# Performance work log

Measured on AMD Instinct MI355X. Metric: run time of the kernel, lower is better.

The kernel has to match this reference:

```python
import jax, jax.numpy as jnp
import numpy as np

EPS = 1e-8
NHEAD = 4
N_ITER = 3


def _ln(x, g, b):
    mu = jnp.mean(x, axis=-1, keepdims=True)
    var = jnp.var(x, axis=-1, keepdims=True)
    return (x - mu) / jnp.sqrt(var + 1e-5) * g + b


def _forward(inputs, eps, init_mu, init_logvar, Wk, Wv, Wq,
             ln_in_g, ln_in_b, ln_slot_g, ln_slot_b, ln_res_g, ln_res_b,
             gru_Wih, gru_Whh, gru_bih, gru_bhh, mlp_W1, mlp_W2, mlp_b2):
    B, N, _ = inputs.shape
    D = init_mu.shape[-1]
    dh = D // NHEAD
    # reparameterized init of the figure representation  [B, D]
    rep = init_mu + jnp.exp(0.5 * init_logvar) * eps
    x = _ln(inputs, ln_in_g, ln_in_b)
    # [B, H, N, dh]; k is pre-scaled by sqrt(nhead) as in the source
    k = (x @ Wk).reshape(B, N, NHEAD, dh).transpose(0, 2, 1, 3) * (NHEAD ** 0.5)
    v = (x @ Wv).reshape(B, N, NHEAD, dh).transpose(0, 2, 1, 3)

    def step(rep):
        q = (_ln(rep, ln_slot_g, ln_slot_b) @ Wq).reshape(B, NHEAD, dh)
        # sigmoid attention, normalized over the patch dim N
        w = jax.nn.sigmoid(jnp.einsum('bhnd,bhd->bhn', k, q)) + EPS
        w = w / jnp.sum(w, axis=2, keepdims=True)          # [B, H, N]
        att = jnp.einsum('bhn,bhnd->bhd', w, v).reshape(B, D)
        # GRUCell(input=att, hidden=rep)
        gi = att @ gru_Wih.T + gru_bih
        gh = rep @ gru_Whh.T + gru_bhh
        ir, iz, ig = jnp.split(gi, 3, axis=-1)
        hr, hz, hg = jnp.split(gh, 3, axis=-1)
        r = jax.nn.sigmoid(ir + hr)
        z = jax.nn.sigmoid(iz + hz)
        g = jnp.tanh(ig + r * hg)
        new = (1.0 - z) * g + z * rep
        # residual MLP
        new = new + jax.nn.relu(_ln(new, ln_res_g, ln_res_b) @ mlp_W1) @ mlp_W2 + mlp_b2
        return new, w

    for _ in range(N_ITER):
        rep, w = step(rep)
    # approx_implicit_grad: one extra step from a detached latent
    rep, w = step(jax.lax.stop_gradient(rep))
    return rep, jnp.sum(w, axis=1)[..., None]   # ([B, D], [B, N, 1])


def setup_inputs() -> dict:
    key = jax.random.key(0)
    ks = jax.random.split(key, 12)
    B, N, Din, D, H = 128, 4096, 256, 256, 1024
    s = lambda f: 1.0 / np.sqrt(f)
    return {
        'inputs': jax.random.normal(ks[0], (B, N, Din), jnp.float32),
        'eps': jax.random.normal(ks[1], (B, D), jnp.float32),
        'init_mu': jax.random.normal(ks[2], (1, D), jnp.float32) * 0.02,
        'init_logvar': jax.random.normal(ks[3], (1, D), jnp.float32) * 0.02,
        'Wk': jax.random.normal(ks[4], (Din, D), jnp.float32) * s(Din),
        'Wv': jax.random.normal(ks[5], (Din, D), jnp.float32) * s(Din),
        'Wq': jax.random.normal(ks[6], (D, D), jnp.float32) * s(D),
        'ln_in_g': jnp.ones((Din,), jnp.float32),
        'ln_in_b': jnp.zeros((Din,), jnp.float32),
        'ln_slot_g': jnp.ones((D,), jnp.float32),
        'ln_slot_b': jnp.zeros((D,), jnp.float32),
        'ln_res_g': jnp.ones((D,), jnp.float32),
        'ln_res_b': jnp.zeros((D,), jnp.float32),
        'gru_Wih': jax.random.normal(ks[7], (3 * D, D), jnp.float32) * s(D),
        'gru_Whh': jax.random.normal(ks[8], (3 * D, D), jnp.float32) * s(D),
        'gru_bih': jnp.zeros((3 * D,), jnp.float32),
        'gru_bhh': jnp.zeros((3 * D,), jnp.float32),
        'mlp_W1': jax.random.normal(ks[9], (D, H), jnp.float32) * s(D),
        'mlp_W2': jax.random.normal(ks[10], (H, D), jnp.float32) * s(H),
        'mlp_b2': jnp.zeros((D,), jnp.float32),
    }


def reference(inputs, eps, init_mu, init_logvar, Wk, Wv, Wq,
              ln_in_g, ln_in_b, ln_slot_g, ln_slot_b, ln_res_g, ln_res_b,
              gru_Wih, gru_Whh, gru_bih, gru_bhh, mlp_W1, mlp_W2, mlp_b2):
    return _forward(inputs, eps, init_mu, init_logvar, Wk, Wv, Wq,
                    ln_in_g, ln_in_b, ln_slot_g, ln_slot_b, ln_res_g, ln_res_b,
                    gru_Wih, gru_Whh, gru_bih, gru_bhh, mlp_W1, mlp_W2, mlp_b2)
```

## Files before the change

kernel.cpp:

```cpp
#include <hip/hip_runtime.h>
#include <hip/hip_bf16.h>

typedef __attribute__((ext_vector_type(2))) float f32x2;
typedef __attribute__((ext_vector_type(8))) unsigned short ushort8;
typedef __attribute__((ext_vector_type(4))) unsigned short ushort4_t;

#define N_    4096

__device__ inline float bf2f(unsigned short u){
  union{unsigned int i; float f;} c; c.i = ((unsigned int)u)<<16; return c.f;
}
__device__ inline unsigned short f2bf(float f){
  union{float f; unsigned int i;} c; c.f = f;
  unsigned int x = c.i;
  return (unsigned short)((x + 0x7fffu + ((x>>16)&1u)) >> 16);
}
__device__ inline float sigm(float s){ return 1.0f/(1.0f+__expf(-s)); }
__device__ inline f32x2 up2(unsigned int w){
  union{unsigned int i; float f;} lo, hi;
  lo.i = w<<16; hi.i = w & 0xffff0000u;
  f32x2 r; r.x = lo.f; r.y = hi.f; return r;
}

__device__ inline float blkSum(float v, float* s4){
  v += __shfl_xor(v,1);  v += __shfl_xor(v,2);  v += __shfl_xor(v,4);
  v += __shfl_xor(v,8);  v += __shfl_xor(v,16); v += __shfl_xor(v,32);
  int lane = threadIdx.x & 63, w = threadIdx.x >> 6;
  __syncthreads();
  if (lane==0) s4[w] = v;
  __syncthreads();
  return s4[0]+s4[1]+s4[2]+s4[3];
}

__device__ inline float blkSum16(float v, float* s16){
  #pragma unroll
  for(int o=1;o<64;o<<=1) v += __shfl_xor(v,o);
  int lane = threadIdx.x & 63, w = threadIdx.x >> 6;
  __syncthreads();
  if (lane==0) s16[w] = v;
  __syncthreads();
  float r = 0.f;
  #pragma unroll
  for(int i=0;i<16;i++) r += s16[i];
  return r;
}

__global__ __launch_bounds__(256) void k_prep(
    const float* __restrict__ Wv, const float* __restrict__ Wih,
    const float* __restrict__ Whh, const float* __restrict__ W1,
    const float* __restrict__ W2, const float* __restrict__ Wq,
    const float* __restrict__ Wk,
    unsigned short* __restrict__ Wvp, unsigned short* __restrict__ Wip,
    unsigned short* __restrict__ Whp, unsigned short* __restrict__ W1p,
    unsigned short* __restrict__ W2p, unsigned short* __restrict__ Wqp,
    unsigned short* __restrict__ Wkp){
  int e = blockIdx.x*256 + threadIdx.x;
  if (e < 65536){
    int i = e&3, j = (e>>2)&255, pk = e>>10;
    Wvp[e] = f2bf(Wv[(4*pk+i)*256 + j]);
    Wqp[e] = f2bf(Wq[(4*pk+i)*256 + j]);
  }
  if (e < 196608){
    int i = e&3, j2 = e>>2;
    int j = j2 % 768, pk = j2 / 768;
    Wip[e] = f2bf(Wih[j*256 + 4*pk+i]);
    Whp[e] = f2bf(Whh[j*256 + 4*pk+i]);
  }
  {
    int i = e&3, j = (e>>2)&1023, pk = e>>12;
    W1p[e] = f2bf(W1[(4*pk+i)*1024 + j]);
  }
  {
    int i = e&3, j = (e>>2)&255, pk = e>>10;
    W2p[e] = f2bf(W2[(4*pk+i)*256 + j]);
  }
  if (e < 65536){
    int i = e&3, hc = (e>>2)&1023, pd = e>>12;
    int h = hc>>8, c = hc&255;
    Wkp[e] = f2bf(Wk[c*256 + h*64 + 4*pd+i]);
  }
}

__global__ __launch_bounds__(256) void k_init(
    const float* __restrict__ eps, const float* __restrict__ mu0,
    const float* __restrict__ lv0, const float* __restrict__ sg,
    const float* __restrict__ sb, const float* __restrict__ Wq,
    const unsigned short* __restrict__ Wkp,
    float* __restrict__ rep, float* __restrict__ p_out){
  __shared__ float s4[4]; __shared__ float xq[256]; __shared__ float q_s[256];
  int b = blockIdx.x, c = threadIdx.x;
  float r0 = mu0[c] + __expf(0.5f*lv0[c]) * eps[b*256+c];
  rep[b*256+c] = r0;
  float mu = blkSum(r0, s4) * (1.0f/256.0f);
  float df = r0 - mu;
  float var = blkSum(df*df, s4) * (1.0f/256.0f);
  float rs = rsqrtf(var + 1e-5f);
  xq[c] = df*rs*sg[c] + sb[c];
  __syncthreads();
  float a0=0,a1=0,a2=0,a3=0;
  for(int k=0;k<256;k+=4){
    a0 += xq[k  ]*Wq[(k  )*256+c];
    a1 += xq[k+1]*Wq[(k+1)*256+c];
    a2 += xq[k+2]*Wq[(k+2)*256+c];
    a3 += xq[k+3]*Wq[(k+3)*256+c];
  }
  q_s[c] = a0+a1+a2+a3;
  __syncthreads();
  #pragma unroll
  for(int h=0;h<4;h++){
    float acc = 0.f;
    for(int pd=0;pd<16;pd++){
      ushort4_t w4 = *reinterpret_cast<const ushort4_t*>(Wkp + ((size_t)pd*1024 + h*256 + c)*4);
      acc += bf2f(w4.x)*q_s[h*64+4*pd  ] + bf2f(w4.y)*q_s[h*64+4*pd+1]
           + bf2f(w4.z)*q_s[h*64+4*pd+2] + bf2f(w4.w)*q_s[h*64+4*pd+3];
    }
    p_out[b*1024 + h*256 + c] = 2.0f*acc;
  }
}

__global__ __launch_bounds__(1024) void k_lnattn(
    const float* __restrict__ in, const float* __restrict__ g,
    const float* __restrict__ bln, const float* __restrict__ p,
    unsigned short* __restrict__ x,
    float* __restrict__ u_part, float* __restrict__ ws_part){
  __shared__ float u_red[8][1024];
  __shared__ float ws_red[16][4];
  int split = blockIdx.x, b = blockIdx.y;
  int tid = threadIdx.x, wid = tid>>6, lane = tid&63;
  int grp = tid>>5, cl = tid&31;
  const float* pb = p + (size_t)b*1024;
  f32x2 pp2[4][4];
  #pragma unroll
  for(int h=0;h<4;h++){
    float4 pa = *reinterpret_cast<const float4*>(pb + h*256 + cl*8);
    float4 pc = *reinterpret_cast<const float4*>(pb + h*256 + cl*8 + 4);
    pp2[h][0] = f32x2{pa.x,pa.y}; pp2[h][1] = f32x2{pa.z,pa.w};
    pp2[h][2] = f32x2{pc.x,pc.y}; pp2[h][3] = f32x2{pc.z,pc.w};
  }
  float gg[8], bb[8];
  {
    float4 a = *reinterpret_cast<const float4*>(g + cl*8);
    float4 c = *reinterpret_cast<const float4*>(g + cl*8 + 4);
    gg[0]=a.x; gg[1]=a.y; gg[2]=a.z; gg[3]=a.w; gg[4]=c.x; gg[5]=c.y; gg[6]=c.z; gg[7]=c.w;
    a = *reinterpret_cast<const float4*>(bln + cl*8);
    c = *reinterpret_cast<const float4*>(bln + cl*8 + 4);
    bb[0]=a.x; bb[1]=a.y; bb[2]=a.z; bb[3]=a.w; bb[4]=c.x; bb[5]=c.y; bb[6]=c.z; bb[7]=c.w;
  }
  f32x2 u[4][4] = {};
  float wsum[4] = {0,0,0,0};
  const float* inb = in + ((size_t)b*N_ + split*2048)*256;
  unsigned short* xb = x + ((size_t)b*N_ + split*2048)*256;
  for(int it=0; it<32; ++it){
    int r0 = it*64 + grp, r1 = r0 + 32;
    float4 a0 = *reinterpret_cast<const float4*>(inb + (size_t)r0*256 + cl*8);
    float4 c0 = *reinterpret_cast<const float4*>(inb + (size_t)r0*256 + cl*8 + 4);
    float4 a1 = *reinterpret_cast<const float4*>(inb + (size_t)r1*256 + cl*8);
    float4 c1 = *reinterpret_cast<const float4*>(inb + (size_t)r1*256 + cl*8 + 4);
    float sm0 = a0.x+a0.y+a0.z+a0.w + c0.x+c0.y+c0.z+c0.w;
    float sq0 = a0.x*a0.x+a0.y*a0.y+a0.z*a0.z+a0.w*a0.w
              + c0.x*c0.x+c0.y*c0.y+c0.z*c0.z+c0.w*c0.w;
    float sm1 = a1.x+a1.y+a1.z+a1.w + c1.x+c1.y+c1.z+c1.w;
    float sq1 = a1.x*a1.x+a1.y*a1.y+a1.z*a1.z+a1.w*a1.w
              + c1.x*c1.x+c1.y*c1.y+c1.z*c1.z+c1.w*c1.w;
    #pragma unroll
    for(int o=1;o<32;o<<=1){
      sm0 += __shfl_xor(sm0,o); sq0 += __shfl_xor(sq0,o);
      sm1 += __shfl_xor(sm1,o); sq1 += __shfl_xor(sq1,o);
    }
    float mu0 = sm0*(1.0f/256.0f);
    float rs0 = rsqrtf(sq0*(1.0f/256.0f) - mu0*mu0 + 1e-5f);
    float mu1 = sm1*(1.0f/256.0f);
    float rs1 = rsqrtf(sq1*(1.0f/256.0f) - mu1*mu1 + 1e-5f);
    f32x2 px0[4], px1[4];
    px0[0].x=(a0.x-mu0)*rs0*gg[0]+bb[0]; px0[0].y=(a0.y-mu0)*rs0*gg[1]+bb[1];
    px0[1].x=(a0.z-mu0)*rs0*gg[2]+bb[2]; px0[1].y=(a0.w-mu0)*rs0*gg[3]+bb[3];
    px0[2].x=(c0.x-mu0)*rs0*gg[4]+bb[4]; px0[2].y=(c0.y-mu0)*rs0*gg[5]+bb[5];
    px0[3].x=(c0.z-mu0)*rs0*gg[6]+bb[6]; px0[3].y=(c0.w-mu0)*rs0*gg[7]+bb[7];
    px1[0].x=(a1.x-mu1)*rs1*gg[0]+bb[0]; px1[0].y=(a1.y-mu1)*rs1*gg[1]+bb[1];
    px1[1].x=(a1.z-mu1)*rs1*gg[2]+bb[2]; px1[1].y=(a1.w-mu1)*rs1*gg[3]+bb[3];
    px1[2].x=(c1.x-mu1)*rs1*gg[4]+bb[4]; px1[2].y=(c1.y-mu1)*rs1*gg[5]+bb[5];
    px1[3].x=(c1.z-mu1)*rs1*gg[6]+bb[6]; px1[3].y=(c1.w-mu1)*rs1*gg[7]+bb[7];
    ushort8 o8;
    o8[0]=f2bf(px0[0].x); o8[1]=f2bf(px0[0].y); o8[2]=f2bf(px0[1].x); o8[3]=f2bf(px0[1].y);
    o8[4]=f2bf(px0[2].x); o8[5]=f2bf(px0[2].y); o8[6]=f2bf(px0[3].x); o8[7]=f2bf(px0[3].y);
    *reinterpret_cast<ushort8*>(xb + (size_t)r0*256 + cl*8) = o8;
    o8[0]=f2bf(px1[0].x); o8[1]=f2bf(px1[0].y); o8[2]=f2bf(px1[1].x); o8[3]=f2bf(px1[1].y);
    o8[4]=f2bf(px1[2].x); o8[5]=f2bf(px1[2].y); o8[6]=f2bf(px1[3].x); o8[7]=f2bf(px1[3].y);
    *reinterpret_cast<ushort8*>(xb + (size_t)r1*256 + cl*8) = o8;
    float w0[4], w1[4];
    #pragma unroll
    for(int h=0;h<4;h++){
      f32x2 da = px0[0]*pp2[h][0] + px0[2]*pp2[h][2];
      f32x2 db = px0[1]*pp2[h][1] + px0[3]*pp2[h][3];
      da += db;
      float d0 = da.x + da.y;
      f32x2 ea = px1[0]*pp2[h][0] + px1[2]*pp2[h][2];
      f32x2 eb = px1[1]*pp2[h][1] + px1[3]*pp2[h][3];
      ea += eb;
      float d1 = ea.x + ea.y;
      #pragma unroll
      for(int o=1;o<32;o<<=1){ d0 += __shfl_xor(d0,o); d1 += __shfl_xor(d1,o); }
      w0[h] = sigm(d0) + 1e-8f;
      w1[h] = sigm(d1) + 1e-8f;
      wsum[h] += w0[h] + w1[h];
    }
    #pragma unroll
    for(int h=0;h<4;h++){
      f32x2 wa; wa.x = w0[h]; wa.y = w0[h];
      f32x2 wb; wb.x = w1[h]; wb.y = w1[h];
      #pragma unroll
      for(int j=0;j<4;j++){ u[h][j] += wa*px0[j]; u[h][j] += wb*px1[j]; }
    }
  }
  #pragma unroll
  for(int h=0;h<4;h++){
    #pragma unroll
    for(int j=0;j<4;j++){
      u[h][j].x += __shfl_xor(u[h][j].x,32);
      u[h][j].y += __shfl_xor(u[h][j].y,32);
    }
    wsum[h] += __shfl_xor(wsum[h],32);
  }
  if (wid < 8 && lane < 32){
    #pragma unroll
    for(int h=0;h<4;h++){
      float4 a; a.x=u[h][0].x; a.y=u[h][0].y; a.z=u[h][1].x; a.w=u[h][1].y;
      float4 c; c.x=u[h][2].x; c.y=u[h][2].y; c.z=u[h][3].x; c.w=u[h][3].y;
      *reinterpret_cast<float4*>(&u_red[wid][h*256 + cl*8    ]) = a;
      *reinterpret_cast<float4*>(&u_red[wid][h*256 + cl*8 + 4]) = c;
    }
  }
  if (lane==0){
    #pragma unroll
    for(int h=0;h<4;h++) ws_red[wid][h] = wsum[h];
  }
  __syncthreads();
  if (wid >= 8 && lane < 32){
    #pragma unroll
    for(int h=0;h<4;h++){
      float4 a = *reinterpret_cast<const float4*>(&u_red[wid-8][h*256 + cl*8]);
      float4 c = *reinterpret_cast<const float4*>(&u_red[wid-8][h*256 + cl*8 + 4]);
      a.x+=u[h][0].x; a.y+=u[h][0].y; a.z+=u[h][1].x; a.w+=u[h][1].y;
      c.x+=u[h][2].x; c.y+=u[h][2].y; c.z+=u[h][3].x; c.w+=u[h][3].y;
      *reinterpret_cast<float4*>(&u_red[wid-8][h*256 + cl*8    ]) = a;
      *reinterpret_cast<float4*>(&u_red[wid-8][h*256 + cl*8 + 4]) = c;
    }
  }
  __syncthreads();
  {
    float s = 0.f;
    #pragma unroll
    for(int w=0;w<8;w++) s += u_red[w][tid];
    u_part[((size_t)split*128 + b)*1024 + tid] = s;
  }
  if (tid < 4){
    float s = 0.f;
    #pragma unroll
    for(int w=0;w<16;w++) s += ws_red[w][tid];
    ws_part[((size_t)split*128 + b)*4 + tid] = s;
  }
}

__global__ __launch_bounds__(1024) void k_attnstep(
    const unsigned short* __restrict__ x,
    const float* __restrict__ u_in, const float* __restrict__ ws_in,
    const float* __restrict__ rep_in, float* __restrict__ rep_out,
    const unsigned short* __restrict__ Wvp, const unsigned short* __restrict__ Wip,
    const unsigned short* __restrict__ Whp, const float* __restrict__ bih,
    const float* __restrict__ bhh, const float* __restrict__ ln_rg,
    const float* __restrict__ ln_rb, const unsigned short* __restrict__ W1p,
    const unsigned short* __restrict__ W2p, const float* __restrict__ b2,
    const float* __restrict__ ln_sg, const float* __restrict__ ln_sb,
    const unsigned short* __restrict__ Wqp, const unsigned short* __restrict__ Wkp,
    float* __restrict__ u_out, float* __restrict__ ws_out,
    float* __restrict__ w_buf, int write_w){
  __shared__ float u_s[1024];
  __shared__ float att_s[256], rep_s[256], ln_s[256], nw_s[256], q_s[256];
  __shared__ float gi_s[768], gh_s[768];
  __shared__ float h1_s[1024], p_s[1024], red_a[1024];
  __shared__ float ws_s[4]; __shared__ float s16[16];
  __shared__ float u_red[8][1024];
  __shared__ float ws_red[16][4];
  int split = blockIdx.x, b = blockIdx.y;
  int tid = threadIdx.x;
  int c = tid & 255, s = tid >> 8;
  {
    u_s[tid] = u_in[(size_t)b*1024 + tid] + u_in[((size_t)128 + b)*1024 + tid];
    if (tid < 4) ws_s[tid] = ws_in[b*4 + tid] + ws_in[(128 + b)*4 + tid];
    if (tid < 256) rep_s[tid] = rep_in[b*256 + tid];
  }
  __syncthreads();
  {
    const float* uh = u_s + (c>>6)*256;
    float a0 = 0.f, a1 = 0.f;
    for(int pk=s*16; pk<s*16+16; pk+=2){
      ushort4_t wa = *reinterpret_cast<const ushort4_t*>(Wvp + ((size_t)pk*256 + c)*4);
      ushort4_t wb = *reinterpret_cast<const ushort4_t*>(Wvp + ((size_t)(pk+1)*256 + c)*4);
      a0 += bf2f(wa.x)*uh[4*pk] + bf2f(wa.y)*uh[4*pk+1]
          + bf2f(wa.z)*uh[4*pk+2] + bf2f(wa.w)*uh[4*pk+3];
      a1 += bf2f(wb.x)*uh[4*pk+4] + bf2f(wb.y)*uh[4*pk+5]
          + bf2f(wb.z)*uh[4*pk+6] + bf2f(wb.w)*uh[4*pk+7];
    }
    red_a[tid] = a0+a1;
  }
  __syncthreads();
  if (tid < 256) att_s[tid] = (red_a[tid]+red_a[256+tid]+red_a[512+tid]+red_a[768+tid]) / ws_s[tid>>6];
  __syncthreads();
  if (tid < 768){
    float gi0=0.f, gi1=0.f, gh0=0.f, gh1=0.f;
    for(int pk=0;pk<64;pk+=2){
      ushort4_t wi0 = *reinterpret_cast<const ushort4_t*>(Wip + ((size_t)pk*768 + tid)*4);
      ushort4_t wh0 = *reinterpret_cast<const ushort4_t*>(Whp + ((size_t)pk*768 + tid)*4);
      ushort4_t wi1 = *reinterpret_cast<const ushort4_t*>(Wip + ((size_t)(pk+1)*768 + tid)*4);
      ushort4_t wh1 = *reinterpret_cast<const ushort4_t*>(Whp + ((size_t)(pk+1)*768 + tid)*4);
      gi0 += bf2f(wi0.x)*att_s[4*pk] + bf2f(wi0.y)*att_s[4*pk+1]
           + bf2f(wi0.z)*att_s[4*pk+2] + bf2f(wi0.w)*att_s[4*pk+3];
      gh0 += bf2f(wh0.x)*rep_s[4*pk] + bf2f(wh0.y)*rep_s[4*pk+1]
           + bf2f(wh0.z)*rep_s[4*pk+2] + bf2f(wh0.w)*rep_s[4*pk+3];
      gi1 += bf2f(wi1.x)*att_s[4*pk+4] + bf2f(wi1.y)*att_s[4*pk+5]
           + bf2f(wi1.z)*att_s[4*pk+6] + bf2f(wi1.w)*att_s[4*pk+7];
      gh1 += bf2f(wh1.x)*rep_s[4*pk+4] + bf2f(wh1.y)*rep_s[4*pk+5]
           + bf2f(wh1.z)*rep_s[4*pk+6] + bf2f(wh1.w)*rep_s[4*pk+7];
    }
    gi_s[tid] = gi0+gi1 + bih[tid];
    gh_s[tid] = gh0+gh1 + bhh[tid];
  }
  __syncthreads();
  if (tid < 256){
    float rr = sigm(gi_s[tid]     + gh_s[tid]);
    float zz = sigm(gi_s[256+tid] + gh_s[256+tid]);
    float t3 = tanhf(gi_s[512+tid] + rr*gh_s[512+tid]);
    nw_s[tid] = (1.f-zz)*t3 + zz*rep_s[tid];
  }
  __syncthreads();
  {
    float v = nw_s[c];
    float mu = blkSum16(v, s16)*(1.0f/1024.0f);
    float df = v - mu;
    float var = blkSum16(df*df, s16)*(1.0f/1024.0f);
    float rs = rsqrtf(var+1e-5f);
    if (s==0) ln_s[c] = df*rs*ln_rg[c]+ln_rb[c];
  }
  __syncthreads();
  {
    float a0 = 0.f, a1 = 0.f;
    for(int pk=0;pk<64;pk+=2){
      ushort4_t wa = *reinterpret_cast<const ushort4_t*>(W1p + ((size_t)pk*1024 + tid)*4);
      ushort4_t wb = *reinterpret_cast<const ushort4_t*>(W1p + ((size_t)(pk+1)*1024 + tid)*4);
      a0 += bf2f(wa.x)*ln_s[4*pk] + bf2f(wa.y)*ln_s[4*pk+1]
          + bf2f(wa.z)*ln_s[4*pk+2] + bf2f(wa.w)*ln_s[4*pk+3];
      a1 += bf2f(wb.x)*ln_s[4*pk+4] + bf2f(wb.y)*ln_s[4*pk+5]
          + bf2f(wb.z)*ln_s[4*pk+6] + bf2f(wb.w)*ln_s[4*pk+7];
    }
    h1_s[tid] = fmaxf(a0+a1, 0.f);
  }
  __syncthreads();
  {
    float a0 = 0.f, a1 = 0.f;
    for(int pk=s*64; pk<s*64+64; pk+=2){
      ushort4_t wa = *reinterpret_cast<const ushort4_t*>(W2p + ((size_t)pk*256 + c)*4);
      ushort4_t wb = *reinterpret_cast<const ushort4_t*>(W2p + ((size_t)(pk+1)*256 + c)*4);
      a0 += bf2f(wa.x)*h1_s[4*pk] + bf2f(wa.y)*h1_s[4*pk+1]
          + bf2f(wa.z)*h1_s[4*pk+2] + bf2f(wa.w)*h1_s[4*pk+3];
      a1 += bf2f(wb.x)*h1_s[4*pk+4] + bf2f(wb.y)*h1_s[4*pk+5]
          + bf2f(wb.z)*h1_s[4*pk+6] + bf2f(wb.w)*h1_s[4*pk+7];
    }
    red_a[tid] = a0+a1;
  }
  __syncthreads();
  if (tid < 256){
    float rn = nw_s[tid] + (red_a[tid]+red_a[256+tid]+red_a[512+tid]+red_a[768+tid]) + b2[tid];
    nw_s[tid] = rn;
    if (split==0) rep_out[b*256+tid] = rn;
  }
  __syncthreads();
  {
    float v = nw_s[c];
    float mu = blkSum16(v, s16)*(1.0f/1024.0f);
    float df = v - mu;
    float var = blkSum16(df*df, s16)*(1.0f/1024.0f);
    float rs = rsqrtf(var+1e-5f);
    if (s==0) ln_s[c] = df*rs*ln_sg[c]+ln_sb[c];
  }
  __syncthreads();
  {
    float a0 = 0.f, a1 = 0.f;
    for(int pk=s*16; pk<s*16+16; pk+=2){
      ushort4_t wa = *reinterpret_cast<const ushort4_t*>(Wqp + ((size_t)pk*256 + c)*4);
      ushort4_t wb = *reinterpret_cast<const ushort4_t*>(Wqp + ((size_t)(pk+1)*256 + c)*4);
      a0 += bf2f(wa.x)*ln_s[4*pk] + bf2f(wa.y)*ln_s[4*pk+1]
          + bf2f(wa.z)*ln_s[4*pk+2] + bf2f(wa.w)*ln_s[4*pk+3];
      a1 += bf2f(wb.x)*ln_s[4*pk+4] + bf2f(wb.y)*ln_s[4*pk+5]
          + bf2f(wb.z)*ln_s[4*pk+6] + bf2f(wb.w)*ln_s[4*pk+7];
    }
    red_a[tid] = a0+a1;
  }
  __syncthreads();
  if (tid < 256) q_s[tid] = red_a[tid]+red_a[256+tid]+red_a[512+tid]+red_a[768+tid];
  __syncthreads();
  {
    int h = tid>>8;
    float a0 = 0.f, a1 = 0.f;
    for(int pd=0;pd<16;pd+=2){
      ushort4_t wa = *reinterpret_cast<const ushort4_t*>(Wkp + ((size_t)pd*1024 + tid)*4);
      ushort4_t wb = *reinterpret_cast<const ushort4_t*>(Wkp + ((size_t)(pd+1)*1024 + tid)*4);
      a0 += bf2f(wa.x)*q_s[h*64+4*pd] + bf2f(wa.y)*q_s[h*64+4*pd+1]
          + bf2f(wa.z)*q_s[h*64+4*pd+2] + bf2f(wa.w)*q_s[h*64+4*pd+3];
      a1 += bf2f(wb.x)*q_s[h*64+4*pd+4] + bf2f(wb.y)*q_s[h*64+4*pd+5]
          + bf2f(wb.z)*q_s[h*64+4*pd+6] + bf2f(wb.w)*q_s[h*64+4*pd+7];
    }
    p_s[tid] = 2.0f*(a0+a1);
  }
  __syncthreads();
  int wid = tid>>6, lane = tid&63;
  int grp = tid>>5, cl = tid&31;
  f32x2 pp2[4][4];
  #pragma unroll
  for(int h=0;h<4;h++)
    #pragma unroll
    for(int j2=0;j2<4;j2++){
      pp2[h][j2].x = p_s[h*256 + cl*8 + j2*2];
      pp2[h][j2].y = p_s[h*256 + cl*8 + j2*2 + 1];
    }
  f32x2 u2[4][4] = {};
  float wsum[4] = {0,0,0,0};
  const unsigned short* xb = x + ((size_t)b*N_ + split*2048)*256;
  for(int it=0; it<32; ++it){
    int r0 = it*64 + grp, r1 = r0 + 32;
    uint4 xa = *reinterpret_cast<const uint4*>(xb + (size_t)r0*256 + cl*8);
    uint4 xc = *reinterpret_cast<const uint4*>(xb + (size_t)r1*256 + cl*8);
    f32x2 x0[4], x1[4];
    x0[0]=up2(xa.x); x0[1]=up2(xa.y); x0[2]=up2(xa.z); x0[3]=up2(xa.w);
    x1[0]=up2(xc.x); x1[1]=up2(xc.y); x1[2]=up2(xc.z); x1[3]=up2(xc.w);
    float w0[4], w1[4];
    #pragma unroll
    for(int h=0;h<4;h++){
      f32x2 da = x0[0]*pp2[h][0] + x0[2]*pp2[h][2];
      f32x2 db = x0[1]*pp2[h][1] + x0[3]*pp2[h][3];
      da += db;
      float d0 = da.x + da.y;
      f32x2 ea = x1[0]*pp2[h][0] + x1[2]*pp2[h][2];
      f32x2 eb = x1[1]*pp2[h][1] + x1[3]*pp2[h][3];
      ea += eb;
      float d1 = ea.x + ea.y;
      #pragma unroll
      for(int o=1;o<32;o<<=1){ d0 += __shfl_xor(d0,o); d1 += __shfl_xor(d1,o); }
      w0[h] = sigm(d0) + 1e-8f;
      w1[h] = sigm(d1) + 1e-8f;
      wsum[h] += w0[h] + w1[h];
    }
    #pragma unroll
    for(int h=0;h<4;h++){
      f32x2 wa; wa.x = w0[h]; wa.y = w0[h];
      f32x2 wb; wb.x = w1[h]; wb.y = w1[h];
      #pragma unroll
      for(int j2=0;j2<4;j2++){ u2[h][j2] += wa*x0[j2]; u2[h][j2] += wb*x1[j2]; }
    }
    if (write_w && cl==0){
      float4 wv; wv.x=w0[0]; wv.y=w0[1]; wv.z=w0[2]; wv.w=w0[3];
      *reinterpret_cast<float4*>(w_buf + ((size_t)b*N_ + split*2048 + r0)*4) = wv;
      float4 wz; wz.x=w1[0]; wz.y=w1[1]; wz.z=w1[2]; wz.w=w1[3];
      *reinterpret_cast<float4*>(w_buf + ((size_t)b*N_ + split*2048 + r1)*4) = wz;
    }
  }
  #pragma unroll
  for(int h=0;h<4;h++){
    #pragma unroll
    for(int j2=0;j2<4;j2++){
      u2[h][j2].x += __shfl_xor(u2[h][j2].x,32);
      u2[h][j2].y += __shfl_xor(u2[h][j2].y,32);
    }
    wsum[h] += __shfl_xor(wsum[h],32);
  }
  __syncthreads();
  if (wid < 8 && lane < 32){
    #pragma unroll
    for(int h=0;h<4;h++){
      float4 a; a.x=u2[h][0].x; a.y=u2[h][0].y; a.z=u2[h][1].x; a.w=u2[h][1].y;
      float4 cc; cc.x=u2[h][2].x; cc.y=u2[h][2].y; cc.z=u2[h][3].x; cc.w=u2[h][3].y;
      *reinterpret_cast<float4*>(&u_red[wid][h*256 + cl*8    ]) = a;
      *reinterpret_cast<float4*>(&u_red[wid][h*256 + cl*8 + 4]) = cc;
    }
  }
  if (lane==0){
    #pragma unroll
    for(int h=0;h<4;h++) ws_red[wid][h] = wsum[h];
  }
  __syncthreads();
  if (wid >= 8 && lane < 32){
    #pragma unroll
    for(int h=0;h<4;h++){
      float4 a = *reinterpret_cast<const float4*>(&u_red[wid-8][h*256 + cl*8]);
      float4 cc = *reinterpret_cast<const float4*>(&u_red[wid-8][h*256 + cl*8 + 4]);
      a.x+=u2[h][0].x; a.y+=u2[h][0].y; a.z+=u2[h][1].x; a.w+=u2[h][1].y;
      cc.x+=u2[h][2].x; cc.y+=u2[h][2].y; cc.z+=u2[h][3].x; cc.w+=u2[h][3].y;
      *reinterpret_cast<float4*>(&u_red[wid-8][h*256 + cl*8    ]) = a;
      *reinterpret_cast<float4*>(&u_red[wid-8][h*256 + cl*8 + 4]) = cc;
    }
  }
  __syncthreads();
  {
    float sm = 0.f;
    #pragma unroll
    for(int w=0;w<8;w++) sm += u_red[w][tid];
    u_out[((size_t)split*128 + b)*1024 + tid] = sm;
  }
  if (tid < 4){
    float sm = 0.f;
    #pragma unroll
    for(int w=0;w<16;w++) sm += ws_red[w][tid];
    ws_out[((size_t)split*128 + b)*4 + tid] = sm;
  }
}

__global__ __launch_bounds__(1024) void k_finstep(
    const float* __restrict__ u_in, const float* __restrict__ ws_in,
    const float* __restrict__ rep_in,
    const unsigned short* __restrict__ Wvp, const unsigned short* __restrict__ Wip,
    const unsigned short* __restrict__ Whp, const float* __restrict__ bih,
    const float* __restrict__ bhh, const float* __restrict__ ln_rg,
    const float* __restrict__ ln_rb, const unsigned short* __restrict__ W1p,
    const unsigned short* __restrict__ W2p, const float* __restrict__ b2,
    float* __restrict__ out_rep, float* __restrict__ wsum_tot){
  __shared__ float u_s[1024];
  __shared__ float att_s[256], rep_s[256], ln_s[256], nw_s[256];
  __shared__ float gi_s[768], gh_s[768];
  __shared__ float h1_s[1024], red_a[1024];
  __shared__ float ws_s[4]; __shared__ float s16[16];
  int b = blockIdx.x;
  int tid = threadIdx.x;
  int c = tid & 255, s = tid >> 8;
  {
    u_s[tid] = u_in[(size_t)b*1024 + tid] + u_in[((size_t)128 + b)*1024 + tid];
    if (tid < 4){
      float w = ws_in[b*4 + tid] + ws_in[(128 + b)*4 + tid];
      ws_s[tid] = w; wsum_tot[b*4 + tid] = w;
    }
    if (tid < 256) rep_s[tid] = rep_in[b*256 + tid];
  }
  __syncthreads();
  {
    const float* uh = u_s + (c>>6)*256;
    float a0 = 0.f, a1 = 0.f;
    for(int pk=s*16; pk<s*16+16; pk+=2){
      ushort4_t wa = *reinterpret_cast<const ushort4_t*>(Wvp + ((size_t)pk*256 + c)*4);
      ushort4_t wb = *reinterpret_cast<const ushort4_t*>(Wvp + ((size_t)(pk+1)*256 + c)*4);
      a0 += bf2f(wa.x)*uh[4*pk] + bf2f(wa.y)*uh[4*pk+1]
          + bf2f(wa.z)*uh[4*pk+2] + bf2f(wa.w)*uh[4*pk+3];
      a1 += bf2f(wb.x)*uh[4*pk+4] + bf2f(wb.y)*uh[4*pk+5]
          + bf2f(wb.z)*uh[4*pk+6] + bf2f(wb.w)*uh[4*pk+7];
    }
    red_a[tid] = a0+a1;
  }
  __syncthreads();
  if (tid < 256) att_s[tid] = (red_a[tid]+red_a[256+tid]+red_a[512+tid]+red_a[768+tid]) / ws_s[tid>>6];
  __syncthreads();
  if (tid < 768){
    float gi0=0.f, gi1=0.f, gh0=0.f, gh1=0.f;
    for(int pk=0;pk<64;pk+=2){
      ushort4_t wi0 = *reinterpret_cast<const ushort4_t*>(Wip + ((size_t)pk*768 + tid)*4);
      ushort4_t wh0 = *reinterpret_cast<const ushort4_t*>(Whp + ((size_t)pk*768 + tid)*4);
      ushort4_t wi1 = *reinterpret_cast<const ushort4_t*>(Wip + ((size_t)(pk+1)*768 + tid)*4);
      ushort4_t wh1 = *reinterpret_cast<const ushort4_t*>(Whp + ((size_t)(pk+1)*768 + tid)*4);
      gi0 += bf2f(wi0.x)*att_s[4*pk] + bf2f(wi0.y)*att_s[4*pk+1]
           + bf2f(wi0.z)*att_s[4*pk+2] + bf2f(wi0.w)*att_s[4*pk+3];
      gh0 += bf2f(wh0.x)*rep_s[4*pk] + bf2f(wh0.y)*rep_s[4*pk+1]
           + bf2f(wh0.z)*rep_s[4*pk+2] + bf2f(wh0.w)*rep_s[4*pk+3];
      gi1 += bf2f(wi1.x)*att_s[4*pk+4] + bf2f(wi1.y)*att_s[4*pk+5]
           + bf2f(wi1.z)*att_s[4*pk+6] + bf2f(wi1.w)*att_s[4*pk+7];
      gh1 += bf2f(wh1.x)*rep_s[4*pk+4] + bf2f(wh1.y)*rep_s[4*pk+5]
           + bf2f(wh1.z)*rep_s[4*pk+6] + bf2f(wh1.w)*rep_s[4*pk+7];
    }
    gi_s[tid] = gi0+gi1 + bih[tid];
    gh_s[tid] = gh0+gh1 + bhh[tid];
  }
  __syncthreads();
  if (tid < 256){
    float rr = sigm(gi_s[tid]     + gh_s[tid]);
    float zz = sigm(gi_s[256+tid] + gh_s[256+tid]);
    float t3 = tanhf(gi_s[512+tid] + rr*gh_s[512+tid]);
    nw_s[tid] = (1.f-zz)*t3 + zz*rep_s[tid];
  }
  __syncthreads();
  {
    float v = nw_s[c];
    float mu = blkSum16(v, s16)*(1.0f/1024.0f);
    float df = v - mu;
    float var = blkSum16(df*df, s16)*(1.0f/1024.0f);
    float rs = rsqrtf(var+1e-5f);
    if (s==0) ln_s[c] = df*rs*ln_rg[c]+ln_rb[c];
  }
  __syncthreads();
  {
    float a0 = 0.f, a1 = 0.f;
    for(int pk=0;pk<64;pk+=2){
      ushort4_t wa = *reinterpret_cast<const ushort4_t*>(W1p + ((size_t)pk*1024 + tid)*4);
      ushort4_t wb = *reinterpret_cast<const ushort4_t*>(W1p + ((size_t)(pk+1)*1024 + tid)*4);
      a0 += bf2f(wa.x)*ln_s[4*pk] + bf2f(wa.y)*ln_s[4*pk+1]
          + bf2f(wa.z)*ln_s[4*pk+2] + bf2f(wa.w)*ln_s[4*pk+3];
      a1 += bf2f(wb.x)*ln_s[4*pk+4] + bf2f(wb.y)*ln_s[4*pk+5]
          + bf2f(wb.z)*ln_s[4*pk+6] + bf2f(wb.w)*ln_s[4*pk+7];
    }
    h1_s[tid] = fmaxf(a0+a1, 0.f);
  }
  __syncthreads();
  {
    float a0 = 0.f, a1 = 0.f;
    for(int pk=s*64; pk<s*64+64; pk+=2){
      ushort4_t wa = *reinterpret_cast<const ushort4_t*>(W2p + ((size_t)pk*256 + c)*4);
      ushort4_t wb = *reinterpret_cast<const ushort4_t*>(W2p + ((size_t)(pk+1)*256 + c)*4);
      a0 += bf2f(wa.x)*h1_s[4*pk] + bf2f(wa.y)*h1_s[4*pk+1]
          + bf2f(wa.z)*h1_s[4*pk+2] + bf2f(wa.w)*h1_s[4*pk+3];
      a1 += bf2f(wb.x)*h1_s[4*pk+4] + bf2f(wb.y)*h1_s[4*pk+5]
          + bf2f(wb.z)*h1_s[4*pk+6] + bf2f(wb.w)*h1_s[4*pk+7];
    }
    red_a[tid] = a0+a1;
  }
  __syncthreads();
  if (tid < 256){
    float rn = nw_s[tid] + (red_a[tid]+red_a[256+tid]+red_a[512+tid]+red_a[768+tid]) + b2[tid];
    out_rep[b*256+tid] = rn;
  }
}

__global__ __launch_bounds__(256) void k_wout(
    const float* __restrict__ w_buf, const float* __restrict__ wsum_tot,
    float* __restrict__ out){
  int idx = blockIdx.x*256 + threadIdx.x;
  int b = idx>>12;
  float4 w4 = *reinterpret_cast<const float4*>(w_buf + (size_t)idx*4);
  out[idx] = w4.x/wsum_tot[b*4+0] + w4.y/wsum_tot[b*4+1]
           + w4.z/wsum_tot[b*4+2] + w4.w/wsum_tot[b*4+3];
}

extern "C" void kernel_launch(void* const* d_in, const int* in_sizes, int n_in,
                              void* d_out, int out_size, void* d_ws, size_t ws_size,
                              hipStream_t stream){
  const float* inputs  = (const float*)d_in[0];
  const float* eps     = (const float*)d_in[1];
  const float* init_mu = (const float*)d_in[2];
  const float* init_lv = (const float*)d_in[3];
  const float* Wk      = (const float*)d_in[4];
  const float* Wv      = (const float*)d_in[5];
  const float* Wq      = (const float*)d_in[6];
  const float* ln_in_g = (const float*)d_in[7];
  const float* ln_in_b = (const float*)d_in[8];
  const float* ln_sg   = (const float*)d_in[9];
  const float* ln_sb   = (const float*)d_in[10];
  const float* ln_rg   = (const float*)d_in[11];
  const float* ln_rb   = (const float*)d_in[12];
  const float* Wih     = (const float*)d_in[13];
  const float* Whh     = (const float*)d_in[14];
  const float* bih     = (const float*)d_in[15];
  const float* bhh     = (const float*)d_in[16];
  const float* W1      = (const float*)d_in[17];
  const float* W2      = (const float*)d_in[18];
  const float* b2      = (const float*)d_in[19];

  char* ws = (char*)d_ws;
  size_t off = 0;
  auto alloc = [&](size_t bytes)->void*{
    void* p = ws + off; off += (bytes + 255) & ~(size_t)255; return p;
  };
  unsigned short* x   = (unsigned short*)alloc((size_t)128*N_*256*2);
  unsigned short* Wvp = (unsigned short*)alloc(65536*2);
  unsigned short* Wip = (unsigned short*)alloc(196608*2);
  unsigned short* Whp = (unsigned short*)alloc(196608*2);
  unsigned short* W1p = (unsigned short*)alloc(262144*2);
  unsigned short* W2p = (unsigned short*)alloc(262144*2);
  unsigned short* Wqp = (unsigned short*)alloc(65536*2);
  unsigned short* Wkp = (unsigned short*)alloc(65536*2);
  float* p0    = (float*)alloc((size_t)128*1024*4);
  float* uA    = (float*)alloc((size_t)2*128*1024*4);
  float* uB    = (float*)alloc((size_t)2*128*1024*4);
  float* wsA   = (float*)alloc(2*128*4*4);
  float* wsB   = (float*)alloc(2*128*4*4);
  float* repA  = (float*)alloc(128*256*4);
  float* repB  = (float*)alloc(128*256*4);
  float* wsum_tot = (float*)alloc(512*4);
  float* w_buf = (float*)alloc((size_t)128*N_*4*4);

  float* out_rep = (float*)d_out;
  float* out_w   = out_rep + 128*256;

  k_prep<<<1024,256,0,stream>>>(Wv,Wih,Whh,W1,W2,Wq,Wk, Wvp,Wip,Whp,W1p,W2p,Wqp,Wkp);
  k_init<<<128,256,0,stream>>>(eps, init_mu, init_lv, ln_sg, ln_sb, Wq, Wkp, repA, p0);
  k_lnattn<<<dim3(2,128),1024,0,stream>>>(inputs, ln_in_g, ln_in_b, p0, x, uA, wsA);
  k_attnstep<<<dim3(2,128),1024,0,stream>>>(x, uA, wsA, repA, repB,
      Wvp,Wip,Whp,bih,bhh,ln_rg,ln_rb,W1p,W2p,b2,ln_sg,ln_sb,Wqp,Wkp,
      uB, wsB, w_buf, 0);
  k_attnstep<<<dim3(2,128),1024,0,stream>>>(x, uB, wsB, repB, repA,
      Wvp,Wip,Whp,bih,bhh,ln_rg,ln_rb,W1p,W2p,b2,ln_sg,ln_sb,Wqp,Wkp,
      uA, wsA, w_buf, 0);
  k_attnstep<<<dim3(2,128),1024,0,stream>>>(x, uA, wsA, repA, repB,
      Wvp,Wip,Whp,bih,bhh,ln_rg,ln_rb,W1p,W2p,b2,ln_sg,ln_sb,Wqp,Wkp,
      uB, wsB, w_buf, 1);
  k_finstep<<<128,1024,0,stream>>>(uB, wsB, repB,
      Wvp,Wip,Whp,bih,bhh,ln_rg,ln_rb,W1p,W2p,b2, out_rep, wsum_tot);
  k_wout<<<2048,256,0,stream>>>(w_buf, wsum_tot, out_w);
}
```

Baseline: 616.3 us.

## Use MFMA bf16 for attention logits and split input LayerNorm into own kernel

```diff
diff --git a/kernel.cpp b/kernel.cpp
--- a/kernel.cpp
+++ b/kernel.cpp
@@ -2,6 +2,8 @@
 #include <hip/hip_bf16.h>
 
 typedef __attribute__((ext_vector_type(2))) float f32x2;
+typedef __attribute__((ext_vector_type(4))) float f32x4;
+typedef __attribute__((ext_vector_type(8))) short short8;
 typedef __attribute__((ext_vector_type(8))) unsigned short ushort8;
 typedef __attribute__((ext_vector_type(4))) unsigned short ushort4_t;
 
@@ -118,151 +120,35 @@
   }
 }
 
-__global__ __launch_bounds__(1024) void k_lnattn(
+__global__ __launch_bounds__(256) void k_ln(
     const float* __restrict__ in, const float* __restrict__ g,
-    const float* __restrict__ bln, const float* __restrict__ p,
-    unsigned short* __restrict__ x,
-    float* __restrict__ u_part, float* __restrict__ ws_part){
-  __shared__ float u_red[8][1024];
-  __shared__ float ws_red[16][4];
-  int split = blockIdx.x, b = blockIdx.y;
-  int tid = threadIdx.x, wid = tid>>6, lane = tid&63;
-  int grp = tid>>5, cl = tid&31;
-  const float* pb = p + (size_t)b*1024;
-  f32x2 pp2[4][4];
-  #pragma unroll
-  for(int h=0;h<4;h++){
-    float4 pa = *reinterpret_cast<const float4*>(pb + h*256 + cl*8);
-    float4 pc = *reinterpret_cast<const float4*>(pb + h*256 + cl*8 + 4);
-    pp2[h][0] = f32x2{pa.x,pa.y}; pp2[h][1] = f32x2{pa.z,pa.w};
-    pp2[h][2] = f32x2{pc.x,pc.y}; pp2[h][3] = f32x2{pc.z,pc.w};
-  }
-  float gg[8], bb[8];
-  {
-    float4 a = *reinterpret_cast<const float4*>(g + cl*8);
-    float4 c = *reinterpret_cast<const float4*>(g + cl*8 + 4);
-    gg[0]=a.x; gg[1]=a.y; gg[2]=a.z; gg[3]=a.w; gg[4]=c.x; gg[5]=c.y; gg[6]=c.z; gg[7]=c.w;
-    a = *reinterpret_cast<const float4*>(bln + cl*8);
-    c = *reinterpret_cast<const float4*>(bln + cl*8 + 4);
-    bb[0]=a.x; bb[1]=a.y; bb[2]=a.z; bb[3]=a.w; bb[4]=c.x; bb[5]=c.y; bb[6]=c.z; bb[7]=c.w;
-  }
-  f32x2 u[4][4] = {};
-  float wsum[4] = {0,0,0,0};
-  const float* inb = in + ((size_t)b*N_ + split*2048)*256;
-  unsigned short* xb = x + ((size_t)b*N_ + split*2048)*256;
-  for(int it=0; it<32; ++it){
-    int r0 = it*64 + grp, r1 = r0 + 32;
-    float4 a0 = *reinterpret_cast<const float4*>(inb + (size_t)r0*256 + cl*8);
-    float4 c0 = *reinterpret_cast<const float4*>(inb + (size_t)r0*256 + cl*8 + 4);
-    float4 a1 = *reinterpret_cast<const float4*>(inb + (size_t)r1*256 + cl*8);
-    float4 c1 = *reinterpret_cast<const float4*>(inb + (size_t)r1*256 + cl*8 + 4);
-    float sm0 = a0.x+a0.y+a0.z+a0.w + c0.x+c0.y+c0.z+c0.w;
-    float sq0 = a0.x*a0.x+a0.y*a0.y+a0.z*a0.z+a0.w*a0.w
-              + c0.x*c0.x+c0.y*c0.y+c0.z*c0.z+c0.w*c0.w;
-    float sm1 = a1.x+a1.y+a1.z+a1.w + c1.x+c1.y+c1.z+c1.w;
-    float sq1 = a1.x*a1.x+a1.y*a1.y+a1.z*a1.z+a1.w*a1.w
-              + c1.x*c1.x+c1.y*c1.y+c1.z*c1.z+c1.w*c1.w;
+    const float* __restrict__ bln, unsigned short* __restrict__ x){
+  int wgid = blockIdx.x*4 + (threadIdx.x>>6);
+  int lane = threadIdx.x & 63;
+  float4 gg = reinterpret_cast<const float4*>(g)[lane];
+  float4 bb = reinterpret_cast<const float4*>(bln)[lane];
+  size_t row0 = (size_t)wgid*64;
+  for(int rr=0; rr<64; ++rr){
+    size_t row = row0 + rr;
+    float4 v = reinterpret_cast<const float4*>(in + row*256)[lane];
+    float sm = v.x+v.y+v.z+v.w;
+    float sq = v.x*v.x+v.y*v.y+v.z*v.z+v.w*v.w;
     #pragma unroll
-    for(int o=1;o<32;o<<=1){
-      sm0 += __shfl_xor(sm0,o); sq0 += __shfl_xor(sq0,o);
-      sm1 += __shfl_xor(sm1,o); sq1 += __shfl_xor(sq1,o);
-    }
-    float mu0 = sm0*(1.0f/256.0f);
-    float rs0 = rsqrtf(sq0*(1.0f/256.0f) - mu0*mu0 + 1e-5f);
-    float mu1 = sm1*(1.0f/256.0f);
-    float rs1 = rsqrtf(sq1*(1.0f/256.0f) - mu1*mu1 + 1e-5f);
-    f32x2 px0[4], px1[4];
-    px0[0].x=(a0.x-mu0)*rs0*gg[0]+bb[0]; px0[0].y=(a0.y-mu0)*rs0*gg[1]+bb[1];
-    px0[1].x=(a0.z-mu0)*rs0*gg[2]+bb[2]; px0[1].y=(a0.w-mu0)*rs0*gg[3]+bb[3];
-    px0[2].x=(c0.x-mu0)*rs0*gg[4]+bb[4]; px0[2].y=(c0.y-mu0)*rs0*gg[5]+bb[5];
-    px0[3].x=(c0.z-mu0)*rs0*gg[6]+bb[6]; px0[3].y=(c0.w-mu0)*rs0*gg[7]+bb[7];
-    px1[0].x=(a1.x-mu1)*rs1*gg[0]+bb[0]; px1[0].y=(a1.y-mu1)*rs1*gg[1]+bb[1];
-    px1[1].x=(a1.z-mu1)*rs1*gg[2]+bb[2]; px1[1].y=(a1.w-mu1)*rs1*gg[3]+bb[3];
-    px1[2].x=(c1.x-mu1)*rs1*gg[4]+bb[4]; px1[2].y=(c1.y-mu1)*rs1*gg[5]+bb[5];
-    px1[3].x=(c1.z-mu1)*rs1*gg[6]+bb[6]; px1[3].y=(c1.w-mu1)*rs1*gg[7]+bb[7];
-    ushort8 o8;
-    o8[0]=f2bf(px0[0].x); o8[1]=f2bf(px0[0].y); o8[2]=f2bf(px0[1].x); o8[3]=f2bf(px0[1].y);
-    o8[4]=f2bf(px0[2].x); o8[5]=f2bf(px0[2].y); o8[6]=f2bf(px0[3].x); o8[7]=f2bf(px0[3].y);
-    *reinterpret_cast<ushort8*>(xb + (size_t)r0*256 + cl*8) = o8;
-    o8[0]=f2bf(px1[0].x); o8[1]=f2bf(px1[0].y); o8[2]=f2bf(px1[1].x); o8[3]=f2bf(px1[1].y);
-    o8[4]=f2bf(px1[2].x); o8[5]=f2bf(px1[2].y); o8[6]=f2bf(px1[3].x); o8[7]=f2bf(px1[3].y);
-    *reinterpret_cast<ushort8*>(xb + (size_t)r1*256 + cl*8) = o8;
-    float w0[4], w1[4];
-    #pragma unroll
-    for(int h=0;h<4;h++){
-      f32x2 da = px0[0]*pp2[h][0] + px0[2]*pp2[h][2];
-      f32x2 db = px0[1]*pp2[h][1] + px0[3]*pp2[h][3];
-      da += db;
-      float d0 = da.x + da.y;
-      f32x2 ea = px1[0]*pp2[h][0] + px1[2]*pp2[h][2];
-      f32x2 eb = px1[1]*pp2[h][1] + px1[3]*pp2[h][3];
-      ea += eb;
-      float d1 = ea.x + ea.y;
-      #pragma unroll
-      for(int o=1;o<32;o<<=1){ d0 += __shfl_xor(d0,o); d1 += __shfl_xor(d1,o); }
-      w0[h] = sigm(d0) + 1e-8f;
-      w1[h] = sigm(d1) + 1e-8f;
-      wsum[h] += w0[h] + w1[h];
-    }
-    #pragma unroll
-    for(int h=0;h<4;h++){
-      f32x2 wa; wa.x = w0[h]; wa.y = w0[h];
-      f32x2 wb; wb.x = w1[h]; wb.y = w1[h];
-      #pragma unroll
-      for(int j=0;j<4;j++){ u[h][j] += wa*px0[j]; u[h][j] += wb*px1[j]; }
-    }
-  }
-  #pragma unroll
-  for(int h=0;h<4;h++){
-    #pragma unroll
-    for(int j=0;j<4;j++){
-      u[h][j].x += __shfl_xor(u[h][j].x,32);
-      u[h][j].y += __shfl_xor(u[h][j].y,32);
-    }
-    wsum[h] += __shfl_xor(wsum[h],32);
-  }
-  if (wid < 8 && lane < 32){
-    #pragma unroll
-    for(int h=0;h<4;h++){
-      float4 a; a.x=u[h][0].x; a.y=u[h][0].y; a.z=u[h][1].x; a.w=u[h][1].y;
-      float4 c; c.x=u[h][2].x; c.y=u[h][2].y; c.z=u[h][3].x; c.w=u[h][3].y;
-      *reinterpret_cast<float4*>(&u_red[wid][h*256 + cl*8    ]) = a;
-      *reinterpret_cast<float4*>(&u_red[wid][h*256 + cl*8 + 4]) = c;
-    }
-  }
-  if (lane==0){
-    #pragma unroll
-    for(int h=0;h<4;h++) ws_red[wid][h] = wsum[h];
-  }
-  __syncthreads();
-  if (wid >= 8 && lane < 32){
-    #pragma unroll
-    for(int h=0;h<4;h++){
-      float4 a = *reinterpret_cast<const float4*>(&u_red[wid-8][h*256 + cl*8]);
-      float4 c = *reinterpret_cast<const float4*>(&u_red[wid-8][h*256 + cl*8 + 4]);
-      a.x+=u[h][0].x; a.y+=u[h][0].y; a.z+=u[h][1].x; a.w+=u[h][1].y;
-      c.x+=u[h][2].x; c.y+=u[h][2].y; c.z+=u[h][3].x; c.w+=u[h][3].y;
-      *reinterpret_cast<float4*>(&u_red[wid-8][h*256 + cl*8    ]) = a;
-      *reinterpret_cast<float4*>(&u_red[wid-8][h*256 + cl*8 + 4]) = c;
-    }
-  }
-  __syncthreads();
-  {
-    float s = 0.f;
-    #pragma unroll
-    for(int w=0;w<8;w++) s += u_red[w][tid];
-    u_part[((size_t)split*128 + b)*1024 + tid] = s;
-  }
-  if (tid < 4){
-    float s = 0.f;
-    #pragma unroll
-    for(int w=0;w<16;w++) s += ws_red[w][tid];
-    ws_part[((size_t)split*128 + b)*4 + tid] = s;
+    for(int o=1;o<64;o<<=1){ sm += __shfl_xor(sm,o); sq += __shfl_xor(sq,o); }
+    float mu = sm*(1.0f/256.0f);
+    float var = sq*(1.0f/256.0f) - mu*mu;
+    float rs = rsqrtf(var + 1e-5f);
+    ushort4_t o4;
+    o4.x = f2bf((v.x-mu)*rs*gg.x + bb.x);
+    o4.y = f2bf((v.y-mu)*rs*gg.y + bb.y);
+    o4.z = f2bf((v.z-mu)*rs*gg.z + bb.z);
+    o4.w = f2bf((v.w-mu)*rs*gg.w + bb.w);
+    reinterpret_cast<ushort4_t*>(x + row*256)[lane] = o4;
   }
 }
 
 __global__ __launch_bounds__(1024) void k_attnstep(
-    const unsigned short* __restrict__ x,
+    const unsigned short* __restrict__ x, const float* __restrict__ p_buf,
     const float* __restrict__ u_in, const float* __restrict__ ws_in,
     const float* __restrict__ rep_in, float* __restrict__ rep_out,
     const unsigned short* __restrict__ Wvp, const unsigned short* __restrict__ Wip,
@@ -273,238 +159,252 @@
     const float* __restrict__ ln_sg, const float* __restrict__ ln_sb,
     const unsigned short* __restrict__ Wqp, const unsigned short* __restrict__ Wkp,
     float* __restrict__ u_out, float* __restrict__ ws_out,
-    float* __restrict__ w_buf, int write_w){
+    float* __restrict__ w_buf, int write_w, int first){
   __shared__ float u_s[1024];
-  __shared__ float att_s[256], rep_s[256], ln_s[256], nw_s[256], q_s[256];
+  __shared__ float att_s[256], rep_s[256], ln_s[256], nw_s[256];
   __shared__ float gi_s[768], gh_s[768];
   __shared__ float h1_s[1024], p_s[1024], red_a[1024];
   __shared__ float ws_s[4]; __shared__ float s16[16];
-  __shared__ float u_red[8][1024];
+  __shared__ unsigned short pT[16*264];
+  __shared__ float w_lds[16][32][4];
+  __shared__ float u_red[4][1024];
   __shared__ float ws_red[16][4];
   int split = blockIdx.x, b = blockIdx.y;
   int tid = threadIdx.x;
   int c = tid & 255, s = tid >> 8;
-  {
+  if (!first){
     u_s[tid] = u_in[(size_t)b*1024 + tid] + u_in[((size_t)128 + b)*1024 + tid];
     if (tid < 4) ws_s[tid] = ws_in[b*4 + tid] + ws_in[(128 + b)*4 + tid];
     if (tid < 256) rep_s[tid] = rep_in[b*256 + tid];
-  }
-  __syncthreads();
-  {
-    const float* uh = u_s + (c>>6)*256;
-    float a0 = 0.f, a1 = 0.f;
-    for(int pk=s*16; pk<s*16+16; pk+=2){
-      ushort4_t wa = *reinterpret_cast<const ushort4_t*>(Wvp + ((size_t)pk*256 + c)*4);
-      ushort4_t wb = *reinterpret_cast<const ushort4_t*>(Wvp + ((size_t)(pk+1)*256 + c)*4);
-      a0 += bf2f(wa.x)*uh[4*pk] + bf2f(wa.y)*uh[4*pk+1]
-          + bf2f(wa.z)*uh[4*pk+2] + bf2f(wa.w)*uh[4*pk+3];
-      a1 += bf2f(wb.x)*uh[4*pk+4] + bf2f(wb.y)*uh[4*pk+5]
-          + bf2f(wb.z)*uh[4*pk+6] + bf2f(wb.w)*uh[4*pk+7];
-    }
-    red_a[tid] = a0+a1;
-  }
-  __syncthreads();
-  if (tid < 256) att_s[tid] = (red_a[tid]+red_a[256+tid]+red_a[512+tid]+red_a[768+tid]) / ws_s[tid>>6];
-  __syncthreads();
-  if (tid < 768){
-    float gi0=0.f, gi1=0.f, gh0=0.f, gh1=0.f;
-    for(int pk=0;pk<64;pk+=2){
-      ushort4_t wi0 = *reinterpret_cast<const ushort4_t*>(Wip + ((size_t)pk*768 + tid)*4);
-      ushort4_t wh0 = *reinterpret_cast<const ushort4_t*>(Whp + ((size_t)pk*768 + tid)*4);
-      ushort4_t wi1 = *reinterpret_cast<const ushort4_t*>(Wip + ((size_t)(pk+1)*768 + tid)*4);
-      ushort4_t wh1 = *reinterpret_cast<const ushort4_t*>(Whp + ((size_t)(pk+1)*768 + tid)*4);
-      gi0 += bf2f(wi0.x)*att_s[4*pk] + bf2f(wi0.y)*att_s[4*pk+1]
-           + bf2f(wi0.z)*att_s[4*pk+2] + bf2f(wi0.w)*att_s[4*pk+3];
-      gh0 += bf2f(wh0.x)*rep_s[4*pk] + bf2f(wh0.y)*rep_s[4*pk+1]
-           + bf2f(wh0.z)*rep_s[4*pk+2] + bf2f(wh0.w)*rep_s[4*pk+3];
-      gi1 += bf2f(wi1.x)*att_s[4*pk+4] + bf2f(wi1.y)*att_s[4*pk+5]
-           + bf2f(wi1.z)*att_s[4*pk+6] + bf2f(wi1.w)*att_s[4*pk+7];
-      gh1 += bf2f(wh1.x)*rep_s[4*pk+4] + bf2f(wh1.y)*rep_s[4*pk+5]
-           + bf2f(wh1.z)*rep_s[4*pk+6] + bf2f(wh1.w)*rep_s[4*pk+7];
-    }
-    gi_s[tid] = gi0+gi1 + bih[tid];
-    gh_s[tid] = gh0+gh1 + bhh[tid];
-  }
-  __syncthreads();
-  if (tid < 256){
-    float rr = sigm(gi_s[tid]     + gh_s[tid]);
-    float zz = sigm(gi_s[256+tid] + gh_s[256+tid]);
-    float t3 = tanhf(gi_s[512+tid] + rr*gh_s[512+tid]);
-    nw_s[tid] = (1.f-zz)*t3 + zz*rep_s[tid];
-  }
-  __syncthreads();
-  {
-    float v = nw_s[c];
-    float mu = blkSum16(v, s16)*(1.0f/1024.0f);
-    float df = v - mu;
-    float var = blkSum16(df*df, s16)*(1.0f/1024.0f);
-    float rs = rsqrtf(var+1e-5f);
-    if (s==0) ln_s[c] = df*rs*ln_rg[c]+ln_rb[c];
-  }
-  __syncthreads();
-  {
-    float a0 = 0.f, a1 = 0.f;
-    for(int pk=0;pk<64;pk+=2){
-      ushort4_t wa = *reinterpret_cast<const ushort4_t*>(W1p + ((size_t)pk*1024 + tid)*4);
-      ushort4_t wb = *reinterpret_cast<const ushort4_t*>(W1p + ((size_t)(pk+1)*1024 + tid)*4);
-      a0 += bf2f(wa.x)*ln_s[4*pk] + bf2f(wa.y)*ln_s[4*pk+1]
-          + bf2f(wa.z)*ln_s[4*pk+2] + bf2f(wa.w)*ln_s[4*pk+3];
-      a1 += bf2f(wb.x)*ln_s[4*pk+4] + bf2f(wb.y)*ln_s[4*pk+5]
-          + bf2f(wb.z)*ln_s[4*pk+6] + bf2f(wb.w)*ln_s[4*pk+7];
-    }
-    h1_s[tid] = fmaxf(a0+a1, 0.f);
-  }
-  __syncthreads();
-  {
-    float a0 = 0.f, a1 = 0.f;
-    for(int pk=s*64; pk<s*64+64; pk+=2){
-      ushort4_t wa = *reinterpret_cast<const ushort4_t*>(W2p + ((size_t)pk*256 + c)*4);
-      ushort4_t wb = *reinterpret_cast<const ushort4_t*>(W2p + ((size_t)(pk+1)*256 + c)*4);
-      a0 += bf2f(wa.x)*h1_s[4*pk] + bf2f(wa.y)*h1_s[4*pk+1]
-          + bf2f(wa.z)*h1_s[4*pk+2] + bf2f(wa.w)*h1_s[4*pk+3];
-      a1 += bf2f(wb.x)*h1_s[4*pk+4] + bf2f(wb.y)*h1_s[4*pk+5]
-          + bf2f(wb.z)*h1_s[4*pk+6] + bf2f(wb.w)*h1_s[4*pk+7];
-    }
-    red_a[tid] = a0+a1;
-  }
-  __syncthreads();
-  if (tid < 256){
-    float rn = nw_s[tid] + (red_a[tid]+red_a[256+tid]+red_a[512+tid]+red_a[768+tid]) + b2[tid];
-    nw_s[tid] = rn;
-    if (split==0) rep_out[b*256+tid] = rn;
-  }
-  __syncthreads();
-  {
-    float v = nw_s[c];
-    float mu = blkSum16(v, s16)*(1.0f/1024.0f);
-    float df = v - mu;
-    float var = blkSum16(df*df, s16)*(1.0f/1024.0f);
-    float rs = rsqrtf(var+1e-5f);
-    if (s==0) ln_s[c] = df*rs*ln_sg[c]+ln_sb[c];
-  }
-  __syncthreads();
-  {
-    float a0 = 0.f, a1 = 0.f;
-    for(int pk=s*16; pk<s*16+16; pk+=2){
-      ushort4_t wa = *reinterpret_cast<const ushort4_t*>(Wqp + ((size_t)pk*256 + c)*4);
-      ushort4_t wb = *reinterpret_cast<const ushort4_t*>(Wqp + ((size_t)(pk+1)*256 + c)*4);
-      a0 += bf2f(wa.x)*ln_s[4*pk] + bf2f(wa.y)*ln_s[4*pk+1]
-          + bf2f(wa.z)*ln_s[4*pk+2] + bf2f(wa.w)*ln_s[4*pk+3];
-      a1 += bf2f(wb.x)*ln_s[4*pk+4] + bf2f(wb.y)*ln_s[4*pk+5]
-          + bf2f(wb.z)*ln_s[4*pk+6] + bf2f(wb.w)*ln_s[4*pk+7];
-    }
-    red_a[tid] = a0+a1;
-  }
-  __syncthreads();
-  if (tid < 256) q_s[tid] = red_a[tid]+red_a[256+tid]+red_a[512+tid]+red_a[768+tid];
-  __syncthreads();
-  {
-    int h = tid>>8;
-    float a0 = 0.f, a1 = 0.f;
-    for(int pd=0;pd<16;pd+=2){
-      ushort4_t wa = *reinterpret_cast<const ushort4_t*>(Wkp + ((size_t)pd*1024 + tid)*4);
-      ushort4_t wb = *reinterpret_cast<const ushort4_t*>(Wkp + ((size_t)(pd+1)*1024 + tid)*4);
-      a0 += bf2f(wa.x)*q_s[h*64+4*pd] + bf2f(wa.y)*q_s[h*64+4*pd+1]
-          + bf2f(wa.z)*q_s[h*64+4*pd+2] + bf2f(wa.w)*q_s[h*64+4*pd+3];
-      a1 += bf2f(wb.x)*q_s[h*64+4*pd+4] + bf2f(wb.y)*q_s[h*64+4*pd+5]
-          + bf2f(wb.z)*q_s[h*64+4*pd+6] + bf2f(wb.w)*q_s[h*64+4*pd+7];
-    }
-    p_s[tid] = 2.0f*(a0+a1);
-  }
-  __syncthreads();
-  int wid = tid>>6, lane = tid&63;
-  int grp = tid>>5, cl = tid&31;
-  f32x2 pp2[4][4];
+    __syncthreads();
+    {
+      const float* uh = u_s + (c>>6)*256;
+      float a0 = 0.f, a1 = 0.f;
+      for(int pk=s*16; pk<s*16+16; pk+=2){
+        ushort4_t wa = *reinterpret_cast<const ushort4_t*>(Wvp + ((size_t)pk*256 + c)*4);
+        ushort4_t wb = *reinterpret_cast<const ushort4_t*>(Wvp + ((size_t)(pk+1)*256 + c)*4);
+        a0 += bf2f(wa.x)*uh[4*pk] + bf2f(wa.y)*uh[4*pk+1]
+            + bf2f(wa.z)*uh[4*pk+2] + bf2f(wa.w)*uh[4*pk+3];
+        a1 += bf2f(wb.x)*uh[4*pk+4] + bf2f(wb.y)*uh[4*pk+5]
+            + bf2f(wb.z)*uh[4*pk+6] + bf2f(wb.w)*uh[4*pk+7];
+      }
+      red_a[tid] = a0+a1;
+    }
+    __syncthreads();
+    if (tid < 256) att_s[tid] = (red_a[tid]+red_a[256+tid]+red_a[512+tid]+red_a[768+tid]) / ws_s[tid>>6];
+    __syncthreads();
+    if (tid < 768){
+      float gi0=0.f, gi1=0.f, gh0=0.f, gh1=0.f;
+      for(int pk=0;pk<64;pk+=2){
+        ushort4_t wi0 = *reinterpret_cast<const ushort4_t*>(Wip + ((size_t)pk*768 + tid)*4);
+        ushort4_t wh0 = *reinterpret_cast<const ushort4_t*>(Whp + ((size_t)pk*768 + tid)*4);
+        ushort4_t wi1 = *reinterpret_cast<const ushort4_t*>(Wip + ((size_t)(pk+1)*768 + tid)*4);
+        ushort4_t wh1 = *reinterpret_cast<const ushort4_t*>(Whp + ((size_t)(pk+1)*768 + tid)*4);
+        gi0 += bf2f(wi0.x)*att_s[4*pk] + bf2f(wi0.y)*att_s[4*pk+1]
+             + bf2f(wi0.z)*att_s[4*pk+2] + bf2f(wi0.w)*att_s[4*pk+3];
+        gh0 += bf2f(wh0.x)*rep_s[4*pk] + bf2f(wh0.y)*rep_s[4*pk+1]
+             + bf2f(wh0.z)*rep_s[4*pk+2] + bf2f(wh0.w)*rep_s[4*pk+3];
+        gi1 += bf2f(wi1.x)*att_s[4*pk+4] + bf2f(wi1.y)*att_s[4*pk+5]
+             + bf2f(wi1.z)*att_s[4*pk+6] + bf2f(wi1.w)*att_s[4*pk+7];
+        gh1 += bf2f(wh1.x)*rep_s[4*pk+4] + bf2f(wh1.y)*rep_s[4*pk+5]
+             + bf2f(wh1.z)*rep_s[4*pk+6] + bf2f(wh1.w)*rep_s[4*pk+7];
+      }
+      gi_s[tid] = gi0+gi1 + bih[tid];
+      gh_s[tid] = gh0+gh1 + bhh[tid];
+    }
+    __syncthreads();
+    if (tid < 256){
+      float rr = sigm(gi_s[tid]     + gh_s[tid]);
+      float zz = sigm(gi_s[256+tid] + gh_s[256+tid]);
+      float t3 = tanhf(gi_s[512+tid] + rr*gh_s[512+tid]);
+      nw_s[tid] = (1.f-zz)*t3 + zz*rep_s[tid];
+    }
+    __syncthreads();
+    {
+      float v = nw_s[c];
+      float mu = blkSum16(v, s16)*(1.0f/1024.0f);
+      float df = v - mu;
+      float var = blkSum16(df*df, s16)*(1.0f/1024.0f);
+      float rs = rsqrtf(var+1e-5f);
+      if (s==0) ln_s[c] = df*rs*ln_rg[c]+ln_rb[c];
+    }
+    __syncthreads();
+    {
+      float a0 = 0.f, a1 = 0.f;
+      for(int pk=0;pk<64;pk+=2){
+        ushort4_t wa = *reinterpret_cast<const ushort4_t*>(W1p + ((size_t)pk*1024 + tid)*4);
+        ushort4_t wb = *reinterpret_cast<const ushort4_t*>(W1p + ((size_t)(pk+1)*1024 + tid)*4);
+        a0 += bf2f(wa.x)*ln_s[4*pk] + bf2f(wa.y)*ln_s[4*pk+1]
+            + bf2f(wa.z)*ln_s[4*pk+2] + bf2f(wa.w)*ln_s[4*pk+3];
+        a1 += bf2f(wb.x)*ln_s[4*pk+4] + bf2f(wb.y)*ln_s[4*pk+5]
+            + bf2f(wb.z)*ln_s[4*pk+6] + bf2f(wb.w)*ln_s[4*pk+7];
+      }
+      h1_s[tid] = fmaxf(a0+a1, 0.f);
+    }
+    __syncthreads();
+    {
+      float a0 = 0.f, a1 = 0.f;
+      for(int pk=s*64; pk<s*64+64; pk+=2){
+        ushort4_t wa = *reinterpret_cast<const ushort4_t*>(W2p + ((size_t)pk*256 + c)*4);
+        ushort4_t wb = *reinterpret_cast<const ushort4_t*>(W2p + ((size_t)(pk+1)*256 + c)*4);
+        a0 += bf2f(wa.x)*h1_s[4*pk] + bf2f(wa.y)*h1_s[4*pk+1]
+            + bf2f(wa.z)*h1_s[4*pk+2] + bf2f(wa.w)*h1_s[4*pk+3];
+        a1 += bf2f(wb.x)*h1_s[4*pk+4] + bf2f(wb.y)*h1_s[4*pk+5]
+            + bf2f(wb.z)*h1_s[4*pk+6] + bf2f(wb.w)*h1_s[4*pk+7];
+      }
+      red_a[tid] = a0+a1;
+    }
+    __syncthreads();
+    if (tid < 256){
+      float rn = nw_s[tid] + (red_a[tid]+red_a[256+tid]+red_a[512+tid]+red_a[768+tid]) + b2[tid];
+      nw_s[tid] = rn;
+      if (split==0) rep_out[b*256+tid] = rn;
+    }
+    __syncthreads();
+    {
+      float v = nw_s[c];
+      float mu = blkSum16(v, s16)*(1.0f/1024.0f);
+      float df = v - mu;
+      float var = blkSum16(df*df, s16)*(1.0f/1024.0f);
+      float rs = rsqrtf(var+1e-5f);
+      if (s==0) ln_s[c] = df*rs*ln_sg[c]+ln_sb[c];
+    }
+    __syncthreads();
+    {
+      float a0 = 0.f, a1 = 0.f;
+      for(int pk=s*16; pk<s*16+16; pk+=2){
+        ushort4_t wa = *reinterpret_cast<const ushort4_t*>(Wqp + ((size_t)pk*256 + c)*4);
+        ushort4_t wb = *reinterpret_cast<const ushort4_t*>(Wqp + ((size_t)(pk+1)*256 + c)*4);
+        a0 += bf2f(wa.x)*ln_s[4*pk] + bf2f(wa.y)*ln_s[4*pk+1]
+            + bf2f(wa.z)*ln_s[4*pk+2] + bf2f(wa.w)*ln_s[4*pk+3];
+        a1 += bf2f(wb.x)*ln_s[4*pk+4] + bf2f(wb.y)*ln_s[4*pk+5]
+            + bf2f(wb.z)*ln_s[4*pk+6] + bf2f(wb.w)*ln_s[4*pk+7];
+      }
+      red_a[tid] = a0+a1;
+    }
+    __syncthreads();
+    if (tid < 256) {
+      float qv = red_a[tid]+red_a[256+tid]+red_a[512+tid]+red_a[768+tid];
+      nw_s[tid] = qv;
+    }
+    __syncthreads();
+    {
+      int h = tid>>8;
+      float a0 = 0.f, a1 = 0.f;
+      for(int pd=0;pd<16;pd+=2){
+        ushort4_t wa = *reinterpret_cast<const ushort4_t*>(Wkp + ((size_t)pd*1024 + tid)*4);
+        ushort4_t wb = *reinterpret_cast<const ushort4_t*>(Wkp + ((size_t)(pd+1)*1024 + tid)*4);
+        a0 += bf2f(wa.x)*nw_s[h*64+4*pd] + bf2f(wa.y)*nw_s[h*64+4*pd+1]
+            + bf2f(wa.z)*nw_s[h*64+4*pd+2] + bf2f(wa.w)*nw_s[h*64+4*pd+3];
+        a1 += bf2f(wb.x)*nw_s[h*64+4*pd+4] + bf2f(wb.y)*nw_s[h*64+4*pd+5]
+            + bf2f(wb.z)*nw_s[h*64+4*pd+6] + bf2f(wb.w)*nw_s[h*64+4*pd+7];
+      }
+      p_s[tid] = 2.0f*(a0+a1);
+    }
+  }
+  for(int i=tid; i<16*264; i+=1024) pT[i] = 0;
+  __syncthreads();
+  {
+    int r = tid>>8, cc = tid&255;
+    float pv = first ? p_buf[(size_t)b*1024 + tid] : p_s[tid];
+    pT[r*264 + cc] = f2bf(pv);
+  }
+  __syncthreads();
+  int lane = tid & 63, wid = tid >> 6;
+  int l15 = lane & 15, l4 = lane >> 4;
+  int cl = lane & 31, g2 = lane >> 5;
+  int h = l15;
+  short8 pf[8];
   #pragma unroll
-  for(int h=0;h<4;h++)
-    #pragma unroll
-    for(int j2=0;j2<4;j2++){
-      pp2[h][j2].x = p_s[h*256 + cl*8 + j2*2];
-      pp2[h][j2].y = p_s[h*256 + cl*8 + j2*2 + 1];
-    }
+  for(int kc=0;kc<8;kc++)
+    pf[kc] = *reinterpret_cast<const short8*>(&pT[l15*264 + kc*32 + l4*8]);
   f32x2 u2[4][4] = {};
   float wsum[4] = {0,0,0,0};
   const unsigned short* xb = x + ((size_t)b*N_ + split*2048)*256;
-  for(int it=0; it<32; ++it){
-    int r0 = it*64 + grp, r1 = r0 + 32;
-    uint4 xa = *reinterpret_cast<const uint4*>(xb + (size_t)r0*256 + cl*8);
-    uint4 xc = *reinterpret_cast<const uint4*>(xb + (size_t)r1*256 + cl*8);
-    f32x2 x0[4], x1[4];
-    x0[0]=up2(xa.x); x0[1]=up2(xa.y); x0[2]=up2(xa.z); x0[3]=up2(xa.w);
-    x1[0]=up2(xc.x); x1[1]=up2(xc.y); x1[2]=up2(xc.z); x1[3]=up2(xc.w);
-    float w0[4], w1[4];
+  for(int it=0; it<4; ++it){
+    int nb = wid*128 + it*32;
+    f32x4 s0 = {}, s1 = {};
     #pragma unroll
-    for(int h=0;h<4;h++){
-      f32x2 da = x0[0]*pp2[h][0] + x0[2]*pp2[h][2];
-      f32x2 db = x0[1]*pp2[h][1] + x0[3]*pp2[h][3];
-      da += db;
-      float d0 = da.x + da.y;
-      f32x2 ea = x1[0]*pp2[h][0] + x1[2]*pp2[h][2];
-      f32x2 eb = x1[1]*pp2[h][1] + x1[3]*pp2[h][3];
-      ea += eb;
-      float d1 = ea.x + ea.y;
+    for(int kc=0;kc<8;kc++){
+      short8 a0 = *reinterpret_cast<const short8*>(xb + (size_t)(nb      + l15)*256 + kc*32 + l4*8);
+      short8 a1 = *reinterpret_cast<const short8*>(xb + (size_t)(nb + 16 + l15)*256 + kc*32 + l4*8);
+      s0 = __builtin_amdgcn_mfma_f32_16x16x32_bf16(a0, pf[kc], s0, 0,0,0);
+      s1 = __builtin_amdgcn_mfma_f32_16x16x32_bf16(a1, pf[kc], s1, 0,0,0);
+    }
+    if (h < 4){
       #pragma unroll
-      for(int o=1;o<32;o<<=1){ d0 += __shfl_xor(d0,o); d1 += __shfl_xor(d1,o); }
-      w0[h] = sigm(d0) + 1e-8f;
-      w1[h] = sigm(d1) + 1e-8f;
-      wsum[h] += w0[h] + w1[h];
-    }
+      for(int r=0;r<4;r++){
+        int r0 = l4*4 + r;
+        float w0 = sigm(s0[r]) + 1e-8f;
+        float w1 = sigm(s1[r]) + 1e-8f;
+        w_lds[wid][r0][h]      = w0;
+        w_lds[wid][16 + r0][h] = w1;
+        if (write_w){
+          int n0 = split*2048 + nb + r0;
+          w_buf[((size_t)b*N_ + n0     )*4 + h] = w0;
+          w_buf[((size_t)b*N_ + n0 + 16)*4 + h] = w1;
+        }
+      }
+    }
+    #pragma unroll 4
+    for(int rp=0; rp<16; ++rp){
+      int rowu = rp*2 + g2;
+      float4 wv = *reinterpret_cast<const float4*>(&w_lds[wid][rowu][0]);
+      uint4 xa = *reinterpret_cast<const uint4*>(xb + (size_t)(nb + rowu)*256 + cl*8);
+      f32x2 xf[4];
+      xf[0]=up2(xa.x); xf[1]=up2(xa.y); xf[2]=up2(xa.z); xf[3]=up2(xa.w);
+      float wh4[4] = {wv.x, wv.y, wv.z, wv.w};
+      #pragma unroll
+      for(int hh=0;hh<4;hh++){
+        f32x2 w2; w2.x = wh4[hh]; w2.y = wh4[hh];
+        #pragma unroll
+        for(int j=0;j<4;j++) u2[hh][j] += w2*xf[j];
+      }
+      wsum[0]+=wv.x; wsum[1]+=wv.y; wsum[2]+=wv.z; wsum[3]+=wv.w;
+    }
+  }
+  #pragma unroll
+  for(int hh=0;hh<4;hh++){
     #pragma unroll
-    for(int h=0;h<4;h++){
-      f32x2 wa; wa.x = w0[h]; wa.y = w0[h];
-      f32x2 wb; wb.x = w1[h]; wb.y = w1[h];
+    for(int j=0;j<4;j++){
+      u2[hh][j].x += __shfl_xor(u2[hh][j].x,32);
+      u2[hh][j].y += __shfl_xor(u2[hh][j].y,32);
+    }
+    wsum[hh] += __shfl_xor(wsum[hh],32);
+  }
+  __syncthreads();
+  if (lane==0){
+    ws_red[wid][0]=wsum[0]; ws_red[wid][1]=wsum[1];
+    ws_red[wid][2]=wsum[2]; ws_red[wid][3]=wsum[3];
+  }
+  if (wid < 4 && lane < 32){
+    #pragma unroll
+    for(int hh=0;hh<4;hh++){
+      float4 a; a.x=u2[hh][0].x; a.y=u2[hh][0].y; a.z=u2[hh][1].x; a.w=u2[hh][1].y;
+      float4 cc; cc.x=u2[hh][2].x; cc.y=u2[hh][2].y; cc.z=u2[hh][3].x; cc.w=u2[hh][3].y;
+      *reinterpret_cast<float4*>(&u_red[wid][hh*256 + cl*8    ]) = a;
+      *reinterpret_cast<float4*>(&u_red[wid][hh*256 + cl*8 + 4]) = cc;
+    }
+  }
+  __syncthreads();
+  #pragma unroll
+  for(int stage=1; stage<4; ++stage){
+    if (wid >= stage*4 && wid < stage*4+4 && lane < 32){
+      int rw = wid - stage*4;
       #pragma unroll
-      for(int j2=0;j2<4;j2++){ u2[h][j2] += wa*x0[j2]; u2[h][j2] += wb*x1[j2]; }
-    }
-    if (write_w && cl==0){
-      float4 wv; wv.x=w0[0]; wv.y=w0[1]; wv.z=w0[2]; wv.w=w0[3];
-      *reinterpret_cast<float4*>(w_buf + ((size_t)b*N_ + split*2048 + r0)*4) = wv;
-      float4 wz; wz.x=w1[0]; wz.y=w1[1]; wz.z=w1[2]; wz.w=w1[3];
-      *reinterpret_cast<float4*>(w_buf + ((size_t)b*N_ + split*2048 + r1)*4) = wz;
-    }
-  }
-  #pragma unroll
-  for(int h=0;h<4;h++){
-    #pragma unroll
-    for(int j2=0;j2<4;j2++){
-      u2[h][j2].x += __shfl_xor(u2[h][j2].x,32);
-      u2[h][j2].y += __shfl_xor(u2[h][j2].y,32);
-    }
-    wsum[h] += __shfl_xor(wsum[h],32);
-  }
-  __syncthreads();
-  if (wid < 8 && lane < 32){
-    #pragma unroll
-    for(int h=0;h<4;h++){
-      float4 a; a.x=u2[h][0].x; a.y=u2[h][0].y; a.z=u2[h][1].x; a.w=u2[h][1].y;
-      float4 cc; cc.x=u2[h][2].x; cc.y=u2[h][2].y; cc.z=u2[h][3].x; cc.w=u2[h][3].y;
-      *reinterpret_cast<float4*>(&u_red[wid][h*256 + cl*8    ]) = a;
-      *reinterpret_cast<float4*>(&u_red[wid][h*256 + cl*8 + 4]) = cc;
-    }
-  }
-  if (lane==0){
-    #pragma unroll
-    for(int h=0;h<4;h++) ws_red[wid][h] = wsum[h];
-  }
-  __syncthreads();
-  if (wid >= 8 && lane < 32){
-    #pragma unroll
-    for(int h=0;h<4;h++){
-      float4 a = *reinterpret_cast<const float4*>(&u_red[wid-8][h*256 + cl*8]);
-      float4 cc = *reinterpret_cast<const float4*>(&u_red[wid-8][h*256 + cl*8 + 4]);
-      a.x+=u2[h][0].x; a.y+=u2[h][0].y; a.z+=u2[h][1].x; a.w+=u2[h][1].y;
-      cc.x+=u2[h][2].x; cc.y+=u2[h][2].y; cc.z+=u2[h][3].x; cc.w+=u2[h][3].y;
-      *reinterpret_cast<float4*>(&u_red[wid-8][h*256 + cl*8    ]) = a;
-      *reinterpret_cast<float4*>(&u_red[wid-8][h*256 + cl*8 + 4]) = cc;
-    }
-  }
-  __syncthreads();
-  {
-    float sm = 0.f;
-    #pragma unroll
-    for(int w=0;w<8;w++) sm += u_red[w][tid];
-    u_out[((size_t)split*128 + b)*1024 + tid] = sm;
-  }
+      for(int hh=0;hh<4;hh++){
+        float4 a = *reinterpret_cast<const float4*>(&u_red[rw][hh*256 + cl*8]);
+        float4 cc = *reinterpret_cast<const float4*>(&u_red[rw][hh*256 + cl*8 + 4]);
+        a.x+=u2[hh][0].x; a.y+=u2[hh][0].y; a.z+=u2[hh][1].x; a.w+=u2[hh][1].y;
+        cc.x+=u2[hh][2].x; cc.y+=u2[hh][2].y; cc.z+=u2[hh][3].x; cc.w+=u2[hh][3].y;
+        *reinterpret_cast<float4*>(&u_red[rw][hh*256 + cl*8    ]) = a;
+        *reinterpret_cast<float4*>(&u_red[rw][hh*256 + cl*8 + 4]) = cc;
+      }
+    }
+    __syncthreads();
+  }
+  u_out[((size_t)split*128 + b)*1024 + tid] =
+      u_red[0][tid]+u_red[1][tid]+u_red[2][tid]+u_red[3][tid];
   if (tid < 4){
     float sm = 0.f;
     #pragma unroll
@@ -685,16 +585,19 @@
 
   k_prep<<<1024,256,0,stream>>>(Wv,Wih,Whh,W1,W2,Wq,Wk, Wvp,Wip,Whp,W1p,W2p,Wqp,Wkp);
   k_init<<<128,256,0,stream>>>(eps, init_mu, init_lv, ln_sg, ln_sb, Wq, Wkp, repA, p0);
-  k_lnattn<<<dim3(2,128),1024,0,stream>>>(inputs, ln_in_g, ln_in_b, p0, x, uA, wsA);
-  k_attnstep<<<dim3(2,128),1024,0,stream>>>(x, uA, wsA, repA, repB,
+  k_ln<<<2048,256,0,stream>>>(inputs, ln_in_g, ln_in_b, x);
+  k_attnstep<<<dim3(2,128),1024,0,stream>>>(x, p0, uA, wsA, repA, repA,
       Wvp,Wip,Whp,bih,bhh,ln_rg,ln_rb,W1p,W2p,b2,ln_sg,ln_sb,Wqp,Wkp,
-      uB, wsB, w_buf, 0);
-  k_attnstep<<<dim3(2,128),1024,0,stream>>>(x, uB, wsB, repB, repA,
+      uA, wsA, w_buf, 0, 1);
+  k_attnstep<<<dim3(2,128),1024,0,stream>>>(x, p0, uA, wsA, repA, repB,
       Wvp,Wip,Whp,bih,bhh,ln_rg,ln_rb,W1p,W2p,b2,ln_sg,ln_sb,Wqp,Wkp,
-      uA, wsA, w_buf, 0);
-  k_attnstep<<<dim3(2,128),1024,0,stream>>>(x, uA, wsA, repA, repB,
+      uB, wsB, w_buf, 0, 0);
+  k_attnstep<<<dim3(2,128),1024,0,stream>>>(x, p0, uB, wsB, repB, repA,
       Wvp,Wip,Whp,bih,bhh,ln_rg,ln_rb,W1p,W2p,b2,ln_sg,ln_sb,Wqp,Wkp,
-      uB, wsB, w_buf, 1);
+      uA, wsA, w_buf, 0, 0);
+  k_attnstep<<<dim3(2,128),1024,0,stream>>>(x, p0, uA, wsA, repA, repB,
+      Wvp,Wip,Whp,bih,bhh,ln_rg,ln_rb,W1p,W2p,b2,ln_sg,ln_sb,Wqp,Wkp,
+      uB, wsB, w_buf, 1, 0);
   k_finstep<<<128,1024,0,stream>>>(uB, wsB, repB,
       Wvp,Wip,Whp,bih,bhh,ln_rg,ln_rb,W1p,W2p,b2, out_rep, wsum_tot);
   k_wout<<<2048,256,0,stream>>>(w_buf, wsum_tot, out_w);
```

Result: slower. 698.9 us (+13.4%).
